# Performance work log

Measured on AMD Instinct MI355X. Metric: run time of the kernel, lower is better.

## Reference

```python
import jax, jax.numpy as jnp
import numpy as np

GRID_H = GRID_W = 17
IMG_H = IMG_W = 128
HFOV = 60.0
ZNEAR, ZFAR = 1.0, 100.0          # FoVPerspectiveCameras defaults
Z_EPS = 0.01                      # MeshRasterizerWithZClamp.z_eps
BLUR_RADIUS = 1e-4
K_FACES = 8                       # faces_per_pixel
SIGMA = 1e-4
GAMMA = 1e-4
BG_COLOR = np.array([0.0, 0.0, 0.0], dtype=np.float32)
Z_BACKGROUND = 100.0


def _build_faces(H, W):
    # Exact replication of the 8 list comprehensions in NovelViewProjector.__init__ (flip=False)
    idx = lambda y, x: y * W + x
    f = []
    for ny in range(0, H - 1, 2):
        for nx in range(1, W - 1, 2):
            f.append([idx(ny, nx + 1), idx(ny, nx), idx(ny + 1, nx)])
    for ny in range(0, H - 1, 2):
        for nx in range(1, W - 1, 2):
            f.append([idx(ny, nx + 1), idx(ny + 1, nx), idx(ny + 1, nx + 1)])
    for ny in range(0, H - 1, 2):
        for nx in range(0, W - 1, 2):
            f.append([idx(ny, nx + 1), idx(ny, nx), idx(ny + 1, nx + 1)])
    for ny in range(0, H - 1, 2):
        for nx in range(0, W - 1, 2):
            f.append([idx(ny + 1, nx + 1), idx(ny, nx), idx(ny + 1, nx)])
    for ny in range(1, H - 1, 2):
        for nx in range(0, W - 1, 2):
            f.append([idx(ny, nx + 1), idx(ny, nx), idx(ny + 1, nx)])
    for ny in range(1, H - 1, 2):
        for nx in range(0, W - 1, 2):
            f.append([idx(ny, nx + 1), idx(ny + 1, nx), idx(ny + 1, nx + 1)])
    for ny in range(1, H - 1, 2):
        for nx in range(1, W - 1, 2):
            f.append([idx(ny, nx + 1), idx(ny, nx), idx(ny + 1, nx + 1)])
    for ny in range(1, H - 1, 2):
        for nx in range(1, W - 1, 2):
            f.append([idx(ny + 1, nx + 1), idx(ny, nx), idx(ny + 1, nx)])
    return np.array(f, dtype=np.int32)


_FACES = _build_faces(GRID_H, GRID_W)                                   # [F,3]
_xs_uv = np.linspace(1, 0, GRID_W)
_ys_uv = np.linspace(0, 1, GRID_H)
_VERTS_UVS = np.array([[x, y] for y in _ys_uv for x in _xs_uv], np.float32)  # [V,2]
_xs = np.linspace(-1, 1, GRID_W)
_ys = np.linspace(-1, 1, GRID_H)
_UNSCALED_GRID = np.array([[x, y] for y in _ys for x in _xs], np.float32)   # [V,2]
_SCALE = np.float32(np.tan(np.deg2rad(HFOV) / 2.0))                     # x_scale = y_scale


def _bilinear(tex, x, y):
    # tex [H,W,3], x/y float pixel coords [P,K] -> [P,K,3]
    H, W = tex.shape[0], tex.shape[1]
    x0f = jnp.clip(jnp.floor(x), 0, W - 1)
    y0f = jnp.clip(jnp.floor(y), 0, H - 1)
    x0 = x0f.astype(jnp.int32)
    y0 = y0f.astype(jnp.int32)
    x1 = jnp.minimum(x0 + 1, W - 1)
    y1 = jnp.minimum(y0 + 1, H - 1)
    wx = (x - x0f)[..., None]
    wy = (y - y0f)[..., None]
    top = (1 - wx) * tex[y0, x0] + wx * tex[y0, x1]
    bot = (1 - wx) * tex[y1, x0] + wx * tex[y1, x1]
    return (1 - wy) * top + wy * bot


def _rasterize_shade(verts_screen, tex):
    # verts_screen [V,3] (ndc xy, view-space z), tex [H,W,3] -> [H,W,5] RGBA+depth
    faces = jnp.asarray(_FACES)
    fv = verts_screen[faces]                 # [F,3,3]
    v2 = fv[:, :, :2]                        # screen xy per face vertex
    zf = fv[:, :, 2]                         # view-space z (z-clamped screen z)
    # pixel NDC grid, pytorch3d convention: +X left, +Y up, row 0 at top
    xs = 1.0 - 2.0 * (jnp.arange(IMG_W, dtype=jnp.float32) + 0.5) / IMG_W
    ys = 1.0 - 2.0 * (jnp.arange(IMG_H, dtype=jnp.float32) + 0.5) / IMG_H
    py, px = jnp.meshgrid(ys, xs, indexing='ij')
    pix = jnp.stack([px.reshape(-1), py.reshape(-1)], -1)       # [P,2]
    a, b, c = v2[:, 0], v2[:, 1], v2[:, 2]                      # [F,2]
    p = pix[:, None, :]                                          # [P,1,2]

    def edge(p, q, r):  # (q-p) x (r-p) -> [P,F]
        return ((q[:, 0] - p[..., 0]) * (r[:, 1] - p[..., 1])
                - (q[:, 1] - p[..., 1]) * (r[:, 0] - p[..., 0]))

    w0 = edge(p, b, c)
    w1 = edge(p, c, a)
    w2 = edge(p, a, b)
    area = (b[:, 0] - a[:, 0]) * (c[:, 1] - a[:, 1]) - (b[:, 1] - a[:, 1]) * (c[:, 0] - a[:, 0])
    area_s = jnp.where(jnp.abs(area) < 1e-8, 1e-8, area)
    bary = jnp.stack([w0, w1, w2], -1) / area_s[None, :, None]   # [P,F,3]
    inside = jnp.all(bary >= 0.0, axis=-1)
    # perspective-correct barycentrics: wi' = wi * prod(z_j, j!=i) / denom
    z0, z1, z2 = zf[:, 0], zf[:, 1], zf[:, 2]
    n0 = bary[..., 0] * z1 * z2
    n1 = bary[..., 1] * z0 * z2
    n2 = bary[..., 2] * z0 * z1
    den = n0 + n1 + n2
    den = jnp.where(jnp.abs(den) < 1e-10, 1e-10, den)
    baryp = jnp.stack([n0, n1, n2], -1) / den[..., None]
    baryc = jnp.clip(baryp, 0.0, None)                           # clip_barycentric_coords
    baryc = baryc / jnp.clip(baryc.sum(-1, keepdims=True), 1e-10, None)
    zpix = jnp.einsum('pfk,fk->pf', baryc, zf)                   # interpolated depth

    def seg_d2(p, s, e):  # squared point-to-segment distance [P,F]
        d = e - s
        t = ((p[..., 0] - s[:, 0]) * d[:, 0] + (p[..., 1] - s[:, 1]) * d[:, 1]) \
            / jnp.clip((d * d).sum(-1), 1e-12, None)
        t = jnp.clip(t, 0.0, 1.0)
        cx = s[:, 0] + t * d[:, 0]
        cy = s[:, 1] + t * d[:, 1]
        return (p[..., 0] - cx) ** 2 + (p[..., 1] - cy) ** 2

    d2 = jnp.minimum(jnp.minimum(seg_d2(p, a, b), seg_d2(p, b, c)), seg_d2(p, c, a))
    sdist = jnp.where(inside, -d2, d2)                           # signed squared dist
    valid = (sdist < BLUR_RADIUS) & (zpix > 1e-4)
    key = jnp.where(valid, zpix, jnp.inf)
    _, idxf = jax.lax.top_k(-key, K_FACES)                       # K nearest faces [P,K]
    take = lambda t: jnp.take_along_axis(t, idxf, axis=1)
    zk = take(zpix)
    dk = take(sdist)
    vk = take(valid.astype(jnp.float32))
    bk = jnp.take_along_axis(baryc, idxf[..., None], axis=1)     # [P,K,3]
    # TexturesUV sampling: interpolate uv, bilinear-sample map (v flipped)
    face_uvs = jnp.asarray(_VERTS_UVS)[faces]                    # [F,3,2]
    uvk = jnp.einsum('pkc,pkcd->pkd', bk, face_uvs[idxf])        # [P,K,2]
    tx = uvk[..., 0] * (tex.shape[1] - 1)
    ty = (1.0 - uvk[..., 1]) * (tex.shape[0] - 1)
    colors = _bilinear(tex, tx, ty)                              # [P,K,3]
    # SoftRGBDShader: softmax rgb blend + z_background depth blend
    prob = jax.nn.sigmoid(-dk / SIGMA) * vk
    alpha = 1.0 - jnp.prod(1.0 - prob, axis=-1)
    zk_s = jnp.where(vk > 0, zk, ZFAR)
    zinv = (ZFAR - zk_s) / (ZFAR - ZNEAR) * vk
    zmax = jnp.clip(zinv.max(-1, keepdims=True), 1e-10, None)
    wnum = prob * jnp.exp((zinv - zmax) / GAMMA)
    delta = jnp.exp((1e-10 - zmax) / GAMMA)                      # background weight [P,1]
    denom = wnum.sum(-1, keepdims=True) + delta
    rgb = (jnp.einsum('pk,pkc->pc', wnum, colors) + delta * jnp.asarray(BG_COLOR)) / denom
    depth = ((wnum * zk_s).sum(-1, keepdims=True) + delta * Z_BACKGROUND) / denom
    out = jnp.concatenate([rgb, alpha[:, None], depth], -1)      # [P,5]
    return out.reshape(IMG_H, IMG_W, 5)


def _forward(xy_offset, z_grid, rgb_in, R_in, T_in, R_out, T_out):
    # vertex un-projection from input view
    scaled_grid = (jnp.asarray(_UNSCALED_GRID) + xy_offset) * _SCALE      # [B,V,2]
    ones = jnp.ones(scaled_grid.shape[:-1] + (1,), scaled_grid.dtype)
    scaled_verts = jnp.concatenate([scaled_grid, ones], -1) * z_grid      # [B,V,3]
    # cam2world (inverse of pytorch3d world->view  v@R + T):  world = (view - T) @ R^T
    verts_world = jnp.einsum('bvj,bkj->bvk', scaled_verts - T_in[:, None, :], R_in)
    # output view transform + FoV perspective projection with z-clamp
    verts_view = jnp.einsum('bvj,bjk->bvk', verts_world, R_out) + T_out[:, None, :]
    s = 1.0 / _SCALE
    z = verts_view[..., 2]
    zden = jnp.where(z >= 0, jnp.maximum(z, Z_EPS), jnp.minimum(z, -Z_EPS))
    verts_screen = jnp.stack([s * verts_view[..., 0] / zden,
                              s * verts_view[..., 1] / zden, z], -1)      # [B,V,3]
    # directly_use_img_as_texture=True -> texture_image_rec = rgb_in
    images = jax.vmap(_rasterize_shade)(verts_screen, rgb_in)             # [B,H,W,5]
    return images


def setup_inputs() -> dict:
    key = jax.random.key(0)
    k1, k2, k3 = jax.random.split(key, 3)
    B, V = 1, GRID_H * GRID_W
    xy_offset = 0.01 * jax.random.normal(k1, (B, V, 2), jnp.float32)
    z_grid = 1.5 + 3.0 * jax.random.uniform(k2, (B, V, 1), jnp.float32)
    rgb_in = jax.random.uniform(k3, (B, IMG_H, IMG_W, 3), jnp.float32)
    R_in = jnp.tile(jnp.eye(3, dtype=jnp.float32)[None], (B, 1, 1))
    T_in = jnp.zeros((B, 3), jnp.float32)
    th = 0.08  # small novel-view rotation about y
    Ry = np.array([[np.cos(th), 0, np.sin(th)], [0, 1, 0], [-np.sin(th), 0, np.cos(th)]], np.float32)
    R_out = jnp.tile(jnp.asarray(Ry)[None], (B, 1, 1))
    T_out = jnp.tile(jnp.asarray(np.array([0.05, 0.0, 0.1], np.float32))[None], (B, 1))
    return {"xy_offset": xy_offset, "z_grid": z_grid, "rgb_in": rgb_in,
            "R_in": R_in, "T_in": T_in, "R_out": R_out, "T_out": T_out}


def reference(xy_offset, z_grid, rgb_in, R_in, T_in, R_out, T_out):
    # returns [B,H,W,5]: rgba = out[...,:4], depth = out[...,4]
    return _forward(xy_offset, z_grid, rgb_in, R_in, T_in, R_out, T_out)
```

## Files before the change

kernel.cpp:

```cpp
#include <hip/hip_runtime.h>
#include <math.h>

#define NVERT 289
#define NFACE 512

__global__ __launch_bounds__(256) void nvp_kernel(
    const float* __restrict__ xy_off,
    const float* __restrict__ z_grid,
    const float* __restrict__ texd,
    const float* __restrict__ R_in,
    const float* __restrict__ T_in,
    const float* __restrict__ R_out,
    const float* __restrict__ T_out,
    float* __restrict__ out)
{
    __shared__ __align__(16) float s_f[NFACE * 28];
    __shared__ float s_vx[NVERT], s_vy[NVERT], s_vz[NVERT];
    __shared__ unsigned char s_flag[NFACE];
    __shared__ int s_list[NFACE];
    __shared__ int s_nf;
    __shared__ float s_tz[4][64][9];
    __shared__ float s_td[4][64][9];
    __shared__ int   s_ti[4][64][9];

    const int tid = threadIdx.x;
    const int tileX = blockIdx.x & 15;
    const int tileY = blockIdx.x >> 4;

    const float SC = 0.57735026918962576f;
    const float SI = 1.0f / 0.57735026918962576f;

    for (int v = tid; v < NVERT; v += 256) {
        int ix = v % 17, iy = v / 17;
        float gx = -1.0f + 0.125f * (float)ix;
        float gy = -1.0f + 0.125f * (float)iy;
        float sx = (gx + xy_off[2 * v]) * SC;
        float sy = (gy + xy_off[2 * v + 1]) * SC;
        float z = z_grid[v];
        float X = sx * z, Y = sy * z, Z = z;
        float p0 = X - T_in[0], p1 = Y - T_in[1], p2 = Z - T_in[2];
        float wxx = R_in[0] * p0 + R_in[1] * p1 + R_in[2] * p2;
        float wyy = R_in[3] * p0 + R_in[4] * p1 + R_in[5] * p2;
        float wzz = R_in[6] * p0 + R_in[7] * p1 + R_in[8] * p2;
        float vx = wxx * R_out[0] + wyy * R_out[3] + wzz * R_out[6] + T_out[0];
        float vy = wxx * R_out[1] + wyy * R_out[4] + wzz * R_out[7] + T_out[1];
        float vz = wxx * R_out[2] + wyy * R_out[5] + wzz * R_out[8] + T_out[2];
        float zden = (vz >= 0.0f) ? fmaxf(vz, 0.01f) : fminf(vz, -0.01f);
        s_vx[v] = SI * vx / zden;
        s_vy[v] = SI * vy / zden;
        s_vz[v] = vz;
    }
    __syncthreads();

    const float pxmax = 1.0f - ((float)(tileX * 8) + 0.5f) * (1.0f / 64.0f);
    const float pxmin = 1.0f - ((float)(tileX * 8) + 7.5f) * (1.0f / 64.0f);
    const float pymax = 1.0f - ((float)(tileY * 8) + 0.5f) * (1.0f / 64.0f);
    const float pymin = 1.0f - ((float)(tileY * 8) + 7.5f) * (1.0f / 64.0f);
    const float MARG = 0.015f;

    for (int f = tid; f < NFACE; f += 256) {
        int g = f >> 6, i = f & 63, rr = i >> 3, cc = i & 7;
        int ny = 2 * rr + (g >> 2);
        int oddx = ((g & 2) ? 0 : 1) ^ (g >> 2);
        int nx = 2 * cc + oddx;
        int p = g & 3;
        const int dy0[4] = {0, 0, 0, 1};
        const int dy1[4] = {0, 1, 0, 0};
        const int dy2[4] = {1, 1, 1, 1};
        const int dx2[4] = {0, 1, 1, 0};
        int v0 = (ny + dy0[p]) * 17 + nx + 1;
        int v1 = (ny + dy1[p]) * 17 + nx;
        int v2 = (ny + dy2[p]) * 17 + nx + dx2[p];

        float ax = s_vx[v0], ay = s_vy[v0], z0 = s_vz[v0];
        float bx = s_vx[v1], by = s_vy[v1], z1 = s_vz[v1];
        float cx = s_vx[v2], cy = s_vy[v2], z2 = s_vz[v2];
        float* F = &s_f[f * 28];
        F[0] = ax; F[1] = ay; F[2] = bx; F[3] = by; F[4] = cx; F[5] = cy;
        float dabx = bx - ax, daby = by - ay;
        F[6] = dabx; F[7] = daby;
        F[8] = 1.0f / fmaxf(dabx * dabx + daby * daby, 1e-12f);
        float dbcx = cx - bx, dbcy = cy - by;
        F[9] = dbcx; F[10] = dbcy;
        F[11] = 1.0f / fmaxf(dbcx * dbcx + dbcy * dbcy, 1e-12f);
        float dcax = ax - cx, dcay = ay - cy;
        F[12] = dcax; F[13] = dcay;
        F[14] = 1.0f / fmaxf(dcax * dcax + dcay * dcay, 1e-12f);
        float area = dabx * (cy - ay) - daby * (cx - ax);
        float areas = (fabsf(area) < 1e-8f) ? 1e-8f : area;
        F[15] = 1.0f / areas;
        F[16] = z0; F[17] = z1; F[18] = z2;
        F[19] = z1 * z2; F[20] = z0 * z2; F[21] = z0 * z1;
        int ix0 = v0 % 17, iy0 = v0 / 17;
        int ix1 = v1 % 17, iy1 = v1 / 17;
        int ix2 = v2 % 17, iy2 = v2 / 17;
        F[22] = 1.0f - 0.0625f * (float)ix0; F[23] = 0.0625f * (float)iy0;
        F[24] = 1.0f - 0.0625f * (float)ix1; F[25] = 0.0625f * (float)iy1;
        F[26] = 1.0f - 0.0625f * (float)ix2; F[27] = 0.0625f * (float)iy2;

        float minx = fminf(ax, fminf(bx, cx)), maxx = fmaxf(ax, fmaxf(bx, cx));
        float miny = fminf(ay, fminf(by, cy)), maxy = fmaxf(ay, fmaxf(by, cy));
        bool ov = (minx - MARG <= pxmax) && (maxx + MARG >= pxmin) &&
                  (miny - MARG <= pymax) && (maxy + MARG >= pymin);
        s_flag[f] = ov ? 1 : 0;
    }
    __syncthreads();

    if (tid < 64) {
        int cnt = 0;
        for (int base = 0; base < NFACE; base += 64) {
            bool ov = s_flag[base + tid] != 0;
            unsigned long long mask = __ballot(ov);
            if (ov) {
                int pos = cnt + (int)__popcll(mask & ((1ull << tid) - 1ull));
                s_list[pos] = base + tid;
            }
            cnt += (int)__popcll(mask);
        }
        if (tid == 0) s_nf = cnt;
    }
    __syncthreads();

    const int p = tid & 63;
    const int sl = tid >> 6;
    const int x = tileX * 8 + (p & 7);
    const int y = tileY * 8 + (p >> 3);
    const float px = 1.0f - ((float)x + 0.5f) * (1.0f / 64.0f);
    const float py = 1.0f - ((float)y + 0.5f) * (1.0f / 64.0f);

    float kk[8], dd[8];
    int ii[8];
#pragma unroll
    for (int j = 0; j < 8; ++j) { kk[j] = __builtin_inff(); dd[j] = 0.0f; ii[j] = -1; }

    const int nf = s_nf;
    for (int i = sl; i < nf; i += 4) {
        const int ci = s_list[i];
        const float4* Fp = (const float4*)(&s_f[ci * 28]);
        const float4 f0 = Fp[0], f1 = Fp[1], f2 = Fp[2], f3 = Fp[3];
        const float ax = f0.x, ay = f0.y, bx = f0.z, by = f0.w, cx = f1.x, cy = f1.y;
        float t, ex, ey, d2;
        t = ((px - ax) * f1.z + (py - ay) * f1.w) * f2.x;
        t = fminf(fmaxf(t, 0.0f), 1.0f);
        ex = px - (ax + t * f1.z); ey = py - (ay + t * f1.w);
        d2 = ex * ex + ey * ey;
        t = ((px - bx) * f2.y + (py - by) * f2.z) * f2.w;
        t = fminf(fmaxf(t, 0.0f), 1.0f);
        ex = px - (bx + t * f2.y); ey = py - (by + t * f2.z);
        d2 = fminf(d2, ex * ex + ey * ey);
        t = ((px - cx) * f3.x + (py - cy) * f3.y) * f3.z;
        t = fminf(fmaxf(t, 0.0f), 1.0f);
        ex = px - (cx + t * f3.x); ey = py - (cy + t * f3.y);
        d2 = fminf(d2, ex * ex + ey * ey);
        float w0 = (bx - px) * (cy - py) - (by - py) * (cx - px);
        float w1 = (cx - px) * (ay - py) - (cy - py) * (ax - px);
        float w2 = (ax - px) * (by - py) - (ay - py) * (bx - px);
        float b0 = w0 * f3.w, b1 = w1 * f3.w, b2 = w2 * f3.w;
        bool inside = (b0 >= 0.0f) && (b1 >= 0.0f) && (b2 >= 0.0f);
        float sd = inside ? -d2 : d2;
        if (sd < 1e-4f) {
            const float4 f4 = Fp[4], f5 = Fp[5];
            float n0 = b0 * f4.w, n1 = b1 * f5.x, n2 = b2 * f5.y;
            float den = n0 + n1 + n2;
            den = (fabsf(den) < 1e-10f) ? 1e-10f : den;
            float c0 = fmaxf(n0 / den, 0.0f);
            float c1 = fmaxf(n1 / den, 0.0f);
            float c2 = fmaxf(n2 / den, 0.0f);
            float scn = fmaxf(c0 + c1 + c2, 1e-10f);
            float zp = (c0 * f4.x + c1 * f4.y + c2 * f4.z) / scn;
            if (zp > 1e-4f && zp < kk[7]) {
#pragma unroll
                for (int j = 7; j >= 1; --j) {
                    bool m1 = zp < kk[j];
                    bool m2 = zp < kk[j - 1];
                    kk[j] = m1 ? (m2 ? kk[j - 1] : zp) : kk[j];
                    dd[j] = m1 ? (m2 ? dd[j - 1] : sd) : dd[j];
                    ii[j] = m1 ? (m2 ? ii[j - 1] : ci) : ii[j];
                }
                if (zp < kk[0]) { kk[0] = zp; dd[0] = sd; ii[0] = ci; }
            }
        }
    }

#pragma unroll
    for (int j = 0; j < 8; ++j) {
        s_tz[sl][p][j] = kk[j];
        s_td[sl][p][j] = dd[j];
        s_ti[sl][p][j] = ii[j];
    }
    __syncthreads();

    if (tid < 64) {
        int h0 = 0, h1 = 0, h2 = 0, h3 = 0;
        float z0h = s_tz[0][tid][0], z1h = s_tz[1][tid][0];
        float z2h = s_tz[2][tid][0], z3h = s_tz[3][tid][0];
        float mk[8], md[8];
        int mi[8];
#pragma unroll
        for (int j = 0; j < 8; ++j) {
            int s01 = (z1h < z0h) ? 1 : 0;
            float za = fminf(z0h, z1h);
            int s23 = (z3h < z2h) ? 3 : 2;
            float zb = fminf(z2h, z3h);
            int sw = (zb < za) ? s23 : s01;
            float zw = fminf(za, zb);
            mk[j] = zw;
            if (sw == 0)      { md[j] = s_td[0][tid][h0]; mi[j] = s_ti[0][tid][h0]; ++h0; z0h = (h0 < 8) ? s_tz[0][tid][h0] : __builtin_inff(); }
            else if (sw == 1) { md[j] = s_td[1][tid][h1]; mi[j] = s_ti[1][tid][h1]; ++h1; z1h = (h1 < 8) ? s_tz[1][tid][h1] : __builtin_inff(); }
            else if (sw == 2) { md[j] = s_td[2][tid][h2]; mi[j] = s_ti[2][tid][h2]; ++h2; z2h = (h2 < 8) ? s_tz[2][tid][h2] : __builtin_inff(); }
            else              { md[j] = s_td[3][tid][h3]; mi[j] = s_ti[3][tid][h3]; ++h3; z3h = (h3 < 8) ? s_tz[3][tid][h3] : __builtin_inff(); }
        }

        float m_ = 1e-10f, S = 0.0f, aR = 0.0f, aG = 0.0f, aB = 0.0f, aD = 0.0f;
        float om = 1.0f;
#pragma unroll
        for (int j = 0; j < 8; ++j) {
            const int ci = mi[j];
            if (ci >= 0) {
                const float4* Fp = (const float4*)(&s_f[ci * 28]);
                const float4 f0 = Fp[0], f1 = Fp[1], f3 = Fp[3], f4 = Fp[4], f5 = Fp[5], f6 = Fp[6];
                const float ax = f0.x, ay = f0.y, bx = f0.z, by = f0.w, cx = f1.x, cy = f1.y;
                float w0 = (bx - px) * (cy - py) - (by - py) * (cx - px);
                float w1 = (cx - px) * (ay - py) - (cy - py) * (ax - px);
                float w2 = (ax - px) * (by - py) - (ay - py) * (bx - px);
                float b0 = w0 * f3.w, b1 = w1 * f3.w, b2 = w2 * f3.w;
                float n0 = b0 * f4.w, n1 = b1 * f5.x, n2 = b2 * f5.y;
                float den = n0 + n1 + n2;
                den = (fabsf(den) < 1e-10f) ? 1e-10f : den;
                float c0 = fmaxf(n0 / den, 0.0f);
                float c1 = fmaxf(n1 / den, 0.0f);
                float c2 = fmaxf(n2 / den, 0.0f);
                float scn = fmaxf(c0 + c1 + c2, 1e-10f);
                float bc0 = c0 / scn, bc1 = c1 / scn, bc2 = c2 / scn;
                float u = bc0 * f5.z + bc1 * f6.x + bc2 * f6.z;
                float v = bc0 * f5.w + bc1 * f6.y + bc2 * f6.w;
                float tx = u * 127.0f;
                float ty = (1.0f - v) * 127.0f;
                float x0f = fminf(fmaxf(floorf(tx), 0.0f), 127.0f);
                float y0f = fminf(fmaxf(floorf(ty), 0.0f), 127.0f);
                int x0 = (int)x0f, y0 = (int)y0f;
                int x1 = (x0 + 1 < 127) ? x0 + 1 : 127;
                int y1 = (y0 + 1 < 127) ? y0 + 1 : 127;
                float wx = tx - x0f, wy = ty - y0f;
                const float* t00 = texd + (y0 * 128 + x0) * 3;
                const float* t01 = texd + (y0 * 128 + x1) * 3;
                const float* t10 = texd + (y1 * 128 + x0) * 3;
                const float* t11 = texd + (y1 * 128 + x1) * 3;
                float r  = (1.0f - wy) * ((1.0f - wx) * t00[0] + wx * t01[0]) + wy * ((1.0f - wx) * t10[0] + wx * t11[0]);
                float gc = (1.0f - wy) * ((1.0f - wx) * t00[1] + wx * t01[1]) + wy * ((1.0f - wx) * t10[1] + wx * t11[1]);
                float bc = (1.0f - wy) * ((1.0f - wx) * t00[2] + wx * t01[2]) + wy * ((1.0f - wx) * t10[2] + wx * t11[2]);
                float prob = 1.0f / (1.0f + expf(md[j] / 1e-4f));
                float zk = mk[j];
                float zi = (100.0f - zk) / 99.0f;
                om *= (1.0f - prob);
                if (zi > m_) {
                    float scl = expf((m_ - zi) / 1e-4f);
                    S *= scl; aR *= scl; aG *= scl; aB *= scl; aD *= scl;
                    m_ = zi;
                }
                float wgt = prob * expf((zi - m_) / 1e-4f);
                S += wgt; aR += wgt * r; aG += wgt * gc; aB += wgt * bc; aD += wgt * zk;
            }
        }
        float delta = expf((1e-10f - m_) / 1e-4f);
        S += delta;
        aD += delta * 100.0f;
        float invS = 1.0f / S;
        const int o = (y * 128 + x) * 5;
        out[o + 0] = aR * invS;
        out[o + 1] = aG * invS;
        out[o + 2] = aB * invS;
        out[o + 3] = 1.0f - om;
        out[o + 4] = aD * invS;
    }
}

extern "C" void kernel_launch(void* const* d_in, const int* in_sizes, int n_in,
                              void* d_out, int out_size, void* d_ws, size_t ws_size,
                              hipStream_t stream) {
    const float* xy_off = (const float*)d_in[0];
    const float* zg     = (const float*)d_in[1];
    const float* rgb    = (const float*)d_in[2];
    const float* R_in   = (const float*)d_in[3];
    const float* T_in   = (const float*)d_in[4];
    const float* R_out  = (const float*)d_in[5];
    const float* T_out  = (const float*)d_in[6];
    float* out = (float*)d_out;
    nvp_kernel<<<dim3(256), dim3(256), 0, stream>>>(xy_off, zg, rgb, R_in, T_in,
                                                    R_out, T_out, out);
}
```

Before: 80.31 us.

## Compute face setup only for tile-overlapping faces and use fast math

Splits face processing into two passes. The first pass computes only bounding boxes and overlap flags. The second builds the full 28-float face records only for compacted overlapping faces, capped at 128 per tile, and stores them contiguously, which removes the index indirection in the raster loop. Divisions are replaced with reciprocal multiplies and expf with __expf. The MAXB cap silently drops faces if a tile overlaps more than 128, and the fast math slightly changes numerics.

```diff
diff --git a/kernel.cpp b/kernel.cpp
--- a/kernel.cpp
+++ b/kernel.cpp
@@ -3,6 +3,21 @@
 
 #define NVERT 289
 #define NFACE 512
+#define MAXB 128
+
+__device__ __forceinline__ void face_verts(int f, int& v0, int& v1, int& v2) {
+    int g = f >> 6, i = f & 63, rr = i >> 3, cc = i & 7;
+    int ny = 2 * rr + (g >> 2);
+    int oddx = ((g & 2) ? 0 : 1) ^ (g >> 2);
+    int nx = 2 * cc + oddx;
+    int p = g & 3;
+    const int dy0[4] = {0, 0, 0, 1};
+    const int dy1[4] = {0, 1, 0, 0};
+    const int dx2[4] = {0, 1, 1, 0};
+    v0 = (ny + dy0[p]) * 17 + nx + 1;
+    v1 = (ny + dy1[p]) * 17 + nx;
+    v2 = (ny + 1) * 17 + nx + dx2[p];
+}
 
 __global__ __launch_bounds__(256) void nvp_kernel(
     const float* __restrict__ xy_off,
@@ -14,10 +29,10 @@
     const float* __restrict__ T_out,
     float* __restrict__ out)
 {
-    __shared__ __align__(16) float s_f[NFACE * 28];
+    __shared__ __align__(16) float s_f[MAXB * 28];
     __shared__ float s_vx[NVERT], s_vy[NVERT], s_vz[NVERT];
     __shared__ unsigned char s_flag[NFACE];
-    __shared__ int s_list[NFACE];
+    __shared__ int s_list[MAXB];
     __shared__ int s_nf;
     __shared__ float s_tz[4][64][9];
     __shared__ float s_td[4][64][9];
@@ -59,23 +74,44 @@
     const float MARG = 0.015f;
 
     for (int f = tid; f < NFACE; f += 256) {
-        int g = f >> 6, i = f & 63, rr = i >> 3, cc = i & 7;
-        int ny = 2 * rr + (g >> 2);
-        int oddx = ((g & 2) ? 0 : 1) ^ (g >> 2);
-        int nx = 2 * cc + oddx;
-        int p = g & 3;
-        const int dy0[4] = {0, 0, 0, 1};
-        const int dy1[4] = {0, 1, 0, 0};
-        const int dy2[4] = {1, 1, 1, 1};
-        const int dx2[4] = {0, 1, 1, 0};
-        int v0 = (ny + dy0[p]) * 17 + nx + 1;
-        int v1 = (ny + dy1[p]) * 17 + nx;
-        int v2 = (ny + dy2[p]) * 17 + nx + dx2[p];
-
+        int v0, v1, v2;
+        face_verts(f, v0, v1, v2);
+        float ax = s_vx[v0], ay = s_vy[v0];
+        float bx = s_vx[v1], by = s_vy[v1];
+        float cx = s_vx[v2], cy = s_vy[v2];
+        float minx = fminf(ax, fminf(bx, cx)), maxx = fmaxf(ax, fmaxf(bx, cx));
+        float miny = fminf(ay, fminf(by, cy)), maxy = fmaxf(ay, fmaxf(by, cy));
+        bool ov = (minx - MARG <= pxmax) && (maxx + MARG >= pxmin) &&
+                  (miny - MARG <= pymax) && (maxy + MARG >= pymin);
+        s_flag[f] = ov ? 1 : 0;
+    }
+    __syncthreads();
+
+    if (tid < 64) {
+        int cnt = 0;
+        for (int base = 0; base < NFACE; base += 64) {
+            bool ov = s_flag[base + tid] != 0;
+            unsigned long long mask = __ballot(ov);
+            if (ov) {
+                int pos = cnt + (int)__popcll(mask & ((1ull << tid) - 1ull));
+                if (pos < MAXB) s_list[pos] = base + tid;
+            }
+            cnt += (int)__popcll(mask);
+        }
+        if (tid == 0) s_nf = (cnt < MAXB) ? cnt : MAXB;
+    }
+    __syncthreads();
+
+    const int nf = s_nf;
+
+    if (tid < nf) {
+        int f = s_list[tid];
+        int v0, v1, v2;
+        face_verts(f, v0, v1, v2);
         float ax = s_vx[v0], ay = s_vy[v0], z0 = s_vz[v0];
         float bx = s_vx[v1], by = s_vy[v1], z1 = s_vz[v1];
         float cx = s_vx[v2], cy = s_vy[v2], z2 = s_vz[v2];
-        float* F = &s_f[f * 28];
+        float* F = &s_f[tid * 28];
         F[0] = ax; F[1] = ay; F[2] = bx; F[3] = by; F[4] = cx; F[5] = cy;
         float dabx = bx - ax, daby = by - ay;
         F[6] = dabx; F[7] = daby;
@@ -97,27 +133,6 @@
         F[22] = 1.0f - 0.0625f * (float)ix0; F[23] = 0.0625f * (float)iy0;
         F[24] = 1.0f - 0.0625f * (float)ix1; F[25] = 0.0625f * (float)iy1;
         F[26] = 1.0f - 0.0625f * (float)ix2; F[27] = 0.0625f * (float)iy2;
-
-        float minx = fminf(ax, fminf(bx, cx)), maxx = fmaxf(ax, fmaxf(bx, cx));
-        float miny = fminf(ay, fminf(by, cy)), maxy = fmaxf(ay, fmaxf(by, cy));
-        bool ov = (minx - MARG <= pxmax) && (maxx + MARG >= pxmin) &&
-                  (miny - MARG <= pymax) && (maxy + MARG >= pymin);
-        s_flag[f] = ov ? 1 : 0;
-    }
-    __syncthreads();
-
-    if (tid < 64) {
-        int cnt = 0;
-        for (int base = 0; base < NFACE; base += 64) {
-            bool ov = s_flag[base + tid] != 0;
-            unsigned long long mask = __ballot(ov);
-            if (ov) {
-                int pos = cnt + (int)__popcll(mask & ((1ull << tid) - 1ull));
-                s_list[pos] = base + tid;
-            }
-            cnt += (int)__popcll(mask);
-        }
-        if (tid == 0) s_nf = cnt;
     }
     __syncthreads();
 
@@ -133,10 +148,8 @@
 #pragma unroll
     for (int j = 0; j < 8; ++j) { kk[j] = __builtin_inff(); dd[j] = 0.0f; ii[j] = -1; }
 
-    const int nf = s_nf;
     for (int i = sl; i < nf; i += 4) {
-        const int ci = s_list[i];
-        const float4* Fp = (const float4*)(&s_f[ci * 28]);
+        const float4* Fp = (const float4*)(&s_f[i * 28]);
         const float4 f0 = Fp[0], f1 = Fp[1], f2 = Fp[2], f3 = Fp[3];
         const float ax = f0.x, ay = f0.y, bx = f0.z, by = f0.w, cx = f1.x, cy = f1.y;
         float t, ex, ey, d2;
@@ -163,11 +176,12 @@
             float n0 = b0 * f4.w, n1 = b1 * f5.x, n2 = b2 * f5.y;
             float den = n0 + n1 + n2;
             den = (fabsf(den) < 1e-10f) ? 1e-10f : den;
-            float c0 = fmaxf(n0 / den, 0.0f);
-            float c1 = fmaxf(n1 / den, 0.0f);
-            float c2 = fmaxf(n2 / den, 0.0f);
-            float scn = fmaxf(c0 + c1 + c2, 1e-10f);
-            float zp = (c0 * f4.x + c1 * f4.y + c2 * f4.z) / scn;
+            float iden = 1.0f / den;
+            float c0 = fmaxf(n0 * iden, 0.0f);
+            float c1 = fmaxf(n1 * iden, 0.0f);
+            float c2 = fmaxf(n2 * iden, 0.0f);
+            float iscn = 1.0f / fmaxf(c0 + c1 + c2, 1e-10f);
+            float zp = (c0 * f4.x + c1 * f4.y + c2 * f4.z) * iscn;
             if (zp > 1e-4f && zp < kk[7]) {
 #pragma unroll
                 for (int j = 7; j >= 1; --j) {
@@ -175,9 +189,9 @@
                     bool m2 = zp < kk[j - 1];
                     kk[j] = m1 ? (m2 ? kk[j - 1] : zp) : kk[j];
                     dd[j] = m1 ? (m2 ? dd[j - 1] : sd) : dd[j];
-                    ii[j] = m1 ? (m2 ? ii[j - 1] : ci) : ii[j];
+                    ii[j] = m1 ? (m2 ? ii[j - 1] : i) : ii[j];
                 }
-                if (zp < kk[0]) { kk[0] = zp; dd[0] = sd; ii[0] = ci; }
+                if (zp < kk[0]) { kk[0] = zp; dd[0] = sd; ii[0] = i; }
             }
         }
     }
@@ -227,11 +241,12 @@
                 float n0 = b0 * f4.w, n1 = b1 * f5.x, n2 = b2 * f5.y;
                 float den = n0 + n1 + n2;
                 den = (fabsf(den) < 1e-10f) ? 1e-10f : den;
-                float c0 = fmaxf(n0 / den, 0.0f);
-                float c1 = fmaxf(n1 / den, 0.0f);
-                float c2 = fmaxf(n2 / den, 0.0f);
-                float scn = fmaxf(c0 + c1 + c2, 1e-10f);
-                float bc0 = c0 / scn, bc1 = c1 / scn, bc2 = c2 / scn;
+                float iden = 1.0f / den;
+                float c0 = fmaxf(n0 * iden, 0.0f);
+                float c1 = fmaxf(n1 * iden, 0.0f);
+                float c2 = fmaxf(n2 * iden, 0.0f);
+                float iscn = 1.0f / fmaxf(c0 + c1 + c2, 1e-10f);
+                float bc0 = c0 * iscn, bc1 = c1 * iscn, bc2 = c2 * iscn;
                 float u = bc0 * f5.z + bc1 * f6.x + bc2 * f6.z;
                 float v = bc0 * f5.w + bc1 * f6.y + bc2 * f6.w;
                 float tx = u * 127.0f;
@@ -249,20 +264,20 @@
                 float r  = (1.0f - wy) * ((1.0f - wx) * t00[0] + wx * t01[0]) + wy * ((1.0f - wx) * t10[0] + wx * t11[0]);
                 float gc = (1.0f - wy) * ((1.0f - wx) * t00[1] + wx * t01[1]) + wy * ((1.0f - wx) * t10[1] + wx * t11[1]);
                 float bc = (1.0f - wy) * ((1.0f - wx) * t00[2] + wx * t01[2]) + wy * ((1.0f - wx) * t10[2] + wx * t11[2]);
-                float prob = 1.0f / (1.0f + expf(md[j] / 1e-4f));
+                float prob = 1.0f / (1.0f + __expf(md[j] * 1e4f));
                 float zk = mk[j];
-                float zi = (100.0f - zk) / 99.0f;
+                float zi = (100.0f - zk) * (1.0f / 99.0f);
                 om *= (1.0f - prob);
                 if (zi > m_) {
-                    float scl = expf((m_ - zi) / 1e-4f);
+                    float scl = __expf((m_ - zi) * 1e4f);
                     S *= scl; aR *= scl; aG *= scl; aB *= scl; aD *= scl;
                     m_ = zi;
                 }
-                float wgt = prob * expf((zi - m_) / 1e-4f);
+                float wgt = prob * __expf((zi - m_) * 1e4f);
                 S += wgt; aR += wgt * r; aG += wgt * gc; aB += wgt * bc; aD += wgt * zk;
             }
         }
-        float delta = expf((1e-10f - m_) / 1e-4f);
+        float delta = __expf((1e-10f - m_) * 1e4f);
         S += delta;
         aD += delta * 100.0f;
         float invS = 1.0f / S;
```

Result: faster. 76.94 us (-4.2%).
